# Kernel optimization log

Hardware: AMD Instinct MI355X
Metric: run time of the kernel (lower is better)

## Reference

```python
import jax, jax.numpy as jnp
import numpy as np

B, S, E, H = 4, 2048, 1024, 16
HD = E // H  # head_dim = 64


def setup_inputs() -> dict:
    key = jax.random.key(0)
    k1, k2, k3, k4 = jax.random.split(key, 4)
    x = jax.random.normal(k1, (B, S, E), dtype=jnp.float32)
    # torch Linear stores weight as (out, in); y = x @ W.T
    w_qkv = jax.random.normal(k2, (3 * E, E), dtype=jnp.float32) * (E ** -0.5)
    w_proj = jax.random.normal(k3, (E, E), dtype=jnp.float32) * (E ** -0.5)
    b_proj = jax.random.normal(k4, (E,), dtype=jnp.float32) * 0.01
    return {"x": x, "w_qkv": w_qkv, "w_proj": w_proj, "b_proj": b_proj}


def reference(x, w_qkv, w_proj, b_proj):
    b, s, e = x.shape
    # fused QKV, then per-head interleaved split (matches view(B,S,H,3*hd).chunk)
    qkv = jnp.einsum('bse,fe->bsf', x, w_qkv).reshape(b, s, H, 3 * HD)
    q, k, v = jnp.split(qkv, 3, axis=-1)  # each (b, s, H, HD)
    scale = HD ** -0.5
    scores = jnp.einsum('bqhd,bkhd->bhqk', q, k) * scale
    causal = jnp.tril(jnp.ones((s, s), dtype=bool))
    scores = jnp.where(causal, scores, jnp.float32(-jnp.inf))
    probs = jax.nn.softmax(scores, axis=-1)
    out = jnp.einsum('bhqk,bkhd->bqhd', probs, v).reshape(b, s, e)
    return jnp.einsum('bse,fe->bsf', out, w_proj) + b_proj
```

## Files before the change

kernel.cpp:

```cpp
#include <hip/hip_runtime.h>

#define Bq   4
#define Sq   2048
#define Eq   1024
#define Hq   16
#define HDq  64
#define Mq   (Bq*Sq)
#define N1q  (3*Eq)
#define Kq   Eq

typedef __bf16 bf16x8 __attribute__((ext_vector_type(8)));
typedef __bf16 bf16x4 __attribute__((ext_vector_type(4)));
typedef float  f32x4  __attribute__((ext_vector_type(4)));
typedef float  f32x16 __attribute__((ext_vector_type(16)));

#define GAS __attribute__((address_space(1)))
#define LAS __attribute__((address_space(3)))

__device__ __forceinline__ void gl2lds16(const void* g, void* l) {
  __builtin_amdgcn_global_load_lds((GAS const void*)g, (LAS void*)l, 16, 0, 0);
}

__device__ __forceinline__ unsigned pack2(float a, float b) {
  union { __bf16 h[2]; unsigned u; } x;
  x.h[0] = (__bf16)a; x.h[1] = (__bf16)b; return x.u;
}

__global__ __launch_bounds__(256) void cvt4(const float* __restrict__ in,
                                            __bf16* __restrict__ out, int n4) {
  int i = blockIdx.x * 256 + threadIdx.x;
  if (i >= n4) return;
  float4 v = ((const float4*)in)[i];
  bf16x4 o = { (__bf16)v.x, (__bf16)v.y, (__bf16)v.z, (__bf16)v.w };
  ((bf16x4*)out)[i] = o;
}

template <int MODE>
__global__ __launch_bounds__(256) void gemm_bt(const __bf16* __restrict__ A,
                                               const __bf16* __restrict__ Bw,
                                               int N, int K,
                                               __bf16* __restrict__ cbf,
                                               const float* __restrict__ bias,
                                               float* __restrict__ cf32) {
  __shared__ __align__(16) __bf16 As[128 * 32];
  __shared__ __align__(16) __bf16 Bs[128 * 32];
  const int tid  = threadIdx.x;
  const int wave = tid >> 6, lane = tid & 63;
  const int quad = lane >> 4, l15 = lane & 15;
  const int wm = wave & 1, wn = wave >> 1;
  const int bm0 = blockIdx.x * 128;
  const int bn0 = blockIdx.y * 128;

  f32x4 acc[4][4] = {};

  const int ar = tid >> 2, ac = (tid & 3) * 8;
  const __bf16* Ag0 = A  + (long)(bm0 + ar) * K + ac;
  const __bf16* Bg0 = Bw + (long)(bn0 + ar) * K + ac;
  __bf16* As0 = As + wave * 512; __bf16* As1 = As + 2048 + wave * 512;
  __bf16* Bs0 = Bs + wave * 512; __bf16* Bs1 = Bs + 2048 + wave * 512;

  for (int kc = 0; kc < K; kc += 32) {
    gl2lds16(Ag0 + kc,          As0);
    gl2lds16(Ag0 + 64 * K + kc, As1);
    gl2lds16(Bg0 + kc,          Bs0);
    gl2lds16(Bg0 + 64 * K + kc, Bs1);
    __syncthreads();

    bf16x8 af[4], bfr[4];
#pragma unroll
    for (int mt = 0; mt < 4; mt++)
      af[mt] = *(const bf16x8*)&As[(wm * 64 + mt * 16 + l15) * 32 + quad * 8];
#pragma unroll
    for (int nt = 0; nt < 4; nt++)
      bfr[nt] = *(const bf16x8*)&Bs[(wn * 64 + nt * 16 + l15) * 32 + quad * 8];
#pragma unroll
    for (int mt = 0; mt < 4; mt++)
#pragma unroll
      for (int nt = 0; nt < 4; nt++)
        acc[mt][nt] = __builtin_amdgcn_mfma_f32_16x16x32_bf16(af[mt], bfr[nt], acc[mt][nt], 0, 0, 0);
    __syncthreads();
  }

#pragma unroll
  for (int nt = 0; nt < 4; nt++) {
    const int n = bn0 + wn * 64 + nt * 16 + l15;
    float bv = 0.f;
    if (MODE == 1) bv = bias[n];
#pragma unroll
    for (int mt = 0; mt < 4; mt++) {
      const int mbase = bm0 + wm * 64 + mt * 16 + quad * 4;
#pragma unroll
      for (int r = 0; r < 4; r++) {
        const long m = mbase + r;
        if (MODE == 0) cbf[m * N + n] = (__bf16)acc[mt][nt][r];
        else           cf32[m * N + n] = acc[mt][nt][r] + bv;
      }
    }
  }
}

__global__ __launch_bounds__(256) void transv(const __bf16* __restrict__ qkv,
                                              __bf16* __restrict__ vt) {
  __shared__ __align__(16) __bf16 T[64 * 64];
  const int tid = threadIdx.x, wave = tid >> 6;
  const int bh = blockIdx.x >> 5, st = blockIdx.x & 31;
  const int b = bh >> 4, h = bh & 15;
  const long gbase = (long)(b * Sq + st * 64 + (tid >> 3)) * N1q + h * 192 + 128 + (tid & 7) * 8;
  gl2lds16(qkv + gbase,                  T + wave * 512);
  gl2lds16(qkv + gbase + (long)32 * N1q, T + 2048 + wave * 512);
  __syncthreads();
  const int d = tid >> 2, s4 = (tid & 3) * 16;
  bf16x8 o0, o1;
#pragma unroll
  for (int j = 0; j < 8; j++) o0[j] = T[(s4 + j) * 64 + d];
#pragma unroll
  for (int j = 0; j < 8; j++) o1[j] = T[(s4 + 8 + j) * 64 + d];
  __bf16* dst = vt + (long)(bh * 64 + d) * Sq + st * 64 + s4;
  *(bf16x8*)dst = o0;
  *(bf16x8*)(dst + 8) = o1;
}

__global__ __launch_bounds__(256, 2) void attn_fwd(const __bf16* __restrict__ qkv,
                                                   const __bf16* __restrict__ vt,
                                                   __bf16* __restrict__ aout) {
  __shared__ __align__(16) __bf16 Ks[128 * 64];
  __shared__ __align__(16) __bf16 Vs[64 * 128];

  const int tid = threadIdx.x;
  const int w = tid >> 6, lane = tid & 63;
  const int c = lane & 31, h = lane >> 5;
  const int bh = blockIdx.x & 63, p = blockIdx.x >> 6;
  const int b = bh >> 4, head = bh & 15;

  const int krr = lane >> 3, kj = lane & 7;
  const int vrr = lane >> 4, vj = lane & 15;
  constexpr float SC2 = 0.18033688011112042f;

  for (int which = 0; which < 2; ++which) {
    const int qt = which ? (15 - p) : p;
    const int q_g = qt * 128 + w * 32 + c;

    bf16x8 qf[4];
    const __bf16* qp = qkv + (long)(b * Sq + q_g) * N1q + head * 192 + h * 8;
#pragma unroll
    for (int kc2 = 0; kc2 < 4; kc2++) qf[kc2] = *(const bf16x8*)(qp + kc2 * 16);

    f32x16 oT[2] = {};
    float m_i = -1e30f, l_i = 0.f;

    const int nk = qt + 1;
    for (int kt = 0; kt < nk; kt++) {
#pragma unroll
      for (int i = 0; i < 4; i++) {
        const int row = w * 32 + i * 8 + krr;
        gl2lds16(qkv + (long)(b * Sq + kt * 128 + row) * N1q + head * 192 + 64
                     + (kj ^ (krr & 7)) * 8,
                 Ks + (w * 32 + i * 8) * 64);
      }
#pragma unroll
      for (int i = 0; i < 4; i++) {
        const int dr = w * 16 + i * 4 + vrr;
        gl2lds16(vt + (long)(bh * 64 + dr) * Sq + kt * 128 + (vj ^ (dr & 7)) * 8,
                 Vs + (w * 16 + i * 4) * 128);
      }
      __syncthreads();

      f32x16 S[4];
#pragma unroll
      for (int nf = 0; nf < 4; nf++) {
        f32x16 z = {};
#pragma unroll
        for (int kc2 = 0; kc2 < 4; kc2++) {
          bf16x8 kf = *(const bf16x8*)&Ks[(nf * 32 + c) * 64 + (((kc2 * 2 + h) ^ (c & 7)) * 8)];
          z = __builtin_amdgcn_mfma_f32_32x32x16_bf16(kf, qf[kc2], z, 0, 0, 0);
        }
        S[nf] = z;
      }

      float mx = -1e30f;
      if (kt == qt) {
#pragma unroll
        for (int nf = 0; nf < 4; nf++)
#pragma unroll
          for (int r = 0; r < 16; r++) {
            const int kcol = kt * 128 + nf * 32 + (r & 3) + 8 * (r >> 2) + 4 * h;
            float s = S[nf][r] * SC2;
            s = (kcol > q_g) ? -1e30f : s;
            S[nf][r] = s; mx = fmaxf(mx, s);
          }
      } else {
#pragma unroll
        for (int nf = 0; nf < 4; nf++)
#pragma unroll
          for (int r = 0; r < 16; r++) {
            float s = S[nf][r] * SC2;
            S[nf][r] = s; mx = fmaxf(mx, s);
          }
      }
      mx = fmaxf(mx, __shfl_xor(mx, 32));
      const float mn = fmaxf(m_i, mx);
      const float alpha = exp2f(m_i - mn);
      m_i = mn;
      float sum = 0.f;
#pragma unroll
      for (int nf = 0; nf < 4; nf++)
#pragma unroll
        for (int r = 0; r < 16; r++) {
          float pv = exp2f(S[nf][r] - mn);
          S[nf][r] = pv; sum += pv;
        }
      sum += __shfl_xor(sum, 32);
      l_i = l_i * alpha + sum;
      oT[0] *= alpha; oT[1] *= alpha;

#pragma unroll
      for (int kc = 0; kc < 8; kc++) {
        const int nf = kc >> 1, base = 8 * (kc & 1);
        const unsigned pa0 = pack2(S[nf][base + 0], S[nf][base + 1]);
        const unsigned pa1 = pack2(S[nf][base + 2], S[nf][base + 3]);
        const unsigned pb0 = pack2(S[nf][base + 4], S[nf][base + 5]);
        const unsigned pb1 = pack2(S[nf][base + 6], S[nf][base + 7]);
        const unsigned ou0 = h ? pb0 : pa0, ou1 = h ? pb1 : pa1;
        const unsigned su0 = h ? pa0 : pb0, su1 = h ? pa1 : pb1;
        const unsigned ru0 = __shfl_xor(su0, 32), ru1 = __shfl_xor(su1, 32);
        union { bf16x8 v; unsigned u[4]; } pf;
        pf.u[0] = h ? ru0 : ou0;
        pf.u[1] = h ? ru1 : ou1;
        pf.u[2] = h ? ou0 : ru0;
        pf.u[3] = h ? ou1 : ru1;
#pragma unroll
        for (int nf2 = 0; nf2 < 2; nf2++) {
          bf16x8 vf = *(const bf16x8*)&Vs[(nf2 * 32 + c) * 128 + (((kc * 2 + h) ^ (c & 7)) * 8)];
          oT[nf2] = __builtin_amdgcn_mfma_f32_32x32x16_bf16(vf, pf.v, oT[nf2], 0, 0, 0);
        }
      }
      __syncthreads();
    }

    const float inv = 1.0f / l_i;
    const long obase = (long)(b * Sq + q_g) * Eq + head * 64;
#pragma unroll
    for (int nf2 = 0; nf2 < 2; nf2++)
#pragma unroll
      for (int g = 0; g < 4; g++) {
        bf16x4 o;
#pragma unroll
        for (int t = 0; t < 4; t++) o[t] = (__bf16)(oT[nf2][g * 4 + t] * inv);
        *(bf16x4*)(aout + obase + nf2 * 32 + 8 * g + 4 * h) = o;
      }
  }
}

extern "C" void kernel_launch(void* const* d_in, const int* in_sizes, int n_in,
                              void* d_out, int out_size, void* d_ws, size_t ws_size,
                              hipStream_t stream) {
  const float* x      = (const float*)d_in[0];
  const float* w_qkv  = (const float*)d_in[1];
  const float* w_proj = (const float*)d_in[2];
  const float* b_proj = (const float*)d_in[3];
  float* out = (float*)d_out;

  char* w = (char*)d_ws;
  __bf16* xb     = (__bf16*)w; w += (size_t)Mq * Kq * 2;
  __bf16* wqkvb  = (__bf16*)w; w += (size_t)N1q * Kq * 2;
  __bf16* wprojb = (__bf16*)w; w += (size_t)Eq * Kq * 2;
  __bf16* qkvb   = (__bf16*)w; w += (size_t)Mq * N1q * 2;
  __bf16* vtb    = (__bf16*)w; w += (size_t)Bq * Hq * HDq * Sq * 2;
  __bf16* attnb  = (__bf16*)w;

  cvt4<<<(Mq * Kq / 4 + 255) / 256, 256, 0, stream>>>(x, xb, Mq * Kq / 4);
  cvt4<<<(N1q * Kq / 4 + 255) / 256, 256, 0, stream>>>(w_qkv, wqkvb, N1q * Kq / 4);
  cvt4<<<(Eq * Kq / 4 + 255) / 256, 256, 0, stream>>>(w_proj, wprojb, Eq * Kq / 4);

  gemm_bt<0><<<dim3(Mq / 128, N1q / 128), 256, 0, stream>>>(xb, wqkvb, N1q, Kq, qkvb, nullptr, nullptr);

  transv<<<Bq * Hq * (Sq / 64), 256, 0, stream>>>(qkvb, vtb);

  attn_fwd<<<64 * 8, 256, 0, stream>>>(qkvb, vtb, attnb);

  gemm_bt<1><<<dim3(Mq / 128, Eq / 128), 256, 0, stream>>>(attnb, wprojb, Eq, Kq, nullptr, b_proj, out);
}
```

Measured before the change: 292.6 us.

## Fold softmax scale into Q weights and launch one attention block per query tile

Scales the Q rows of the QKV weight during the fp32-to-bf16 conversion by the softmax scale times log2(e), which removes the per-score multiply inside the attention loop. The attention kernel now launches one block per query tile (1024 blocks) instead of pairing tiles p and 15-p in one block, and launch bounds allow 4 blocks per CU. The max and sum reductions are split into two chains for more ILP, and the P-fragment shuffle selection is simplified. The risks are load imbalance from causal tiles of very different lengths, register pressure under the tighter launch bound, and slightly different rounding because Q is scaled before the bf16 cast.

New measurement: 347.7 us. 18.8% more time.

```diff
diff --git a/kernel.cpp b/kernel.cpp
--- a/kernel.cpp
+++ b/kernel.cpp
@@ -32,6 +32,18 @@
   if (i >= n4) return;
   float4 v = ((const float4*)in)[i];
   bf16x4 o = { (__bf16)v.x, (__bf16)v.y, (__bf16)v.z, (__bf16)v.w };
+  ((bf16x4*)out)[i] = o;
+}
+
+__global__ __launch_bounds__(256) void cvt_wqkv(const float* __restrict__ in,
+                                                __bf16* __restrict__ out, int n4) {
+  int i = blockIdx.x * 256 + threadIdx.x;
+  if (i >= n4) return;
+  const int f = i >> 8;
+  const float sc = ((f % 192) < 64) ? 0.18033688011112042f : 1.0f;
+  float4 v = ((const float4*)in)[i];
+  bf16x4 o = { (__bf16)(v.x * sc), (__bf16)(v.y * sc),
+               (__bf16)(v.z * sc), (__bf16)(v.w * sc) };
   ((bf16x4*)out)[i] = o;
 }
 
@@ -120,7 +132,7 @@
   *(bf16x8*)(dst + 8) = o1;
 }
 
-__global__ __launch_bounds__(256, 2) void attn_fwd(const __bf16* __restrict__ qkv,
+__global__ __launch_bounds__(256, 4) void attn_fwd(const __bf16* __restrict__ qkv,
                                                    const __bf16* __restrict__ vt,
                                                    __bf16* __restrict__ aout) {
   __shared__ __align__(16) __bf16 Ks[128 * 64];
@@ -129,126 +141,121 @@
   const int tid = threadIdx.x;
   const int w = tid >> 6, lane = tid & 63;
   const int c = lane & 31, h = lane >> 5;
-  const int bh = blockIdx.x & 63, p = blockIdx.x >> 6;
+  const int bh = blockIdx.x & 63, qt = blockIdx.x >> 6;
   const int b = bh >> 4, head = bh & 15;
 
   const int krr = lane >> 3, kj = lane & 7;
   const int vrr = lane >> 4, vj = lane & 15;
-  constexpr float SC2 = 0.18033688011112042f;
-
-  for (int which = 0; which < 2; ++which) {
-    const int qt = which ? (15 - p) : p;
-    const int q_g = qt * 128 + w * 32 + c;
-
-    bf16x8 qf[4];
-    const __bf16* qp = qkv + (long)(b * Sq + q_g) * N1q + head * 192 + h * 8;
-#pragma unroll
-    for (int kc2 = 0; kc2 < 4; kc2++) qf[kc2] = *(const bf16x8*)(qp + kc2 * 16);
-
-    f32x16 oT[2] = {};
-    float m_i = -1e30f, l_i = 0.f;
-
-    const int nk = qt + 1;
-    for (int kt = 0; kt < nk; kt++) {
-#pragma unroll
-      for (int i = 0; i < 4; i++) {
-        const int row = w * 32 + i * 8 + krr;
-        gl2lds16(qkv + (long)(b * Sq + kt * 128 + row) * N1q + head * 192 + 64
-                     + (kj ^ (krr & 7)) * 8,
-                 Ks + (w * 32 + i * 8) * 64);
-      }
-#pragma unroll
-      for (int i = 0; i < 4; i++) {
-        const int dr = w * 16 + i * 4 + vrr;
-        gl2lds16(vt + (long)(bh * 64 + dr) * Sq + kt * 128 + (vj ^ (dr & 7)) * 8,
-                 Vs + (w * 16 + i * 4) * 128);
-      }
-      __syncthreads();
-
-      f32x16 S[4];
-#pragma unroll
-      for (int nf = 0; nf < 4; nf++) {
-        f32x16 z = {};
-#pragma unroll
-        for (int kc2 = 0; kc2 < 4; kc2++) {
-          bf16x8 kf = *(const bf16x8*)&Ks[(nf * 32 + c) * 64 + (((kc2 * 2 + h) ^ (c & 7)) * 8)];
-          z = __builtin_amdgcn_mfma_f32_32x32x16_bf16(kf, qf[kc2], z, 0, 0, 0);
+
+  const int q_g = qt * 128 + w * 32 + c;
+
+  bf16x8 qf[4];
+  const __bf16* qp = qkv + (long)(b * Sq + q_g) * N1q + head * 192 + h * 8;
+#pragma unroll
+  for (int kc2 = 0; kc2 < 4; kc2++) qf[kc2] = *(const bf16x8*)(qp + kc2 * 16);
+
+  f32x16 oT[2] = {};
+  float m_i = -1e30f, l_i = 0.f;
+
+  const int nk = qt + 1;
+  for (int kt = 0; kt < nk; kt++) {
+#pragma unroll
+    for (int i = 0; i < 4; i++) {
+      const int row = w * 32 + i * 8 + krr;
+      gl2lds16(qkv + (long)(b * Sq + kt * 128 + row) * N1q + head * 192 + 64
+                   + (kj ^ (krr & 7)) * 8,
+               Ks + (w * 32 + i * 8) * 64);
+    }
+#pragma unroll
+    for (int i = 0; i < 4; i++) {
+      const int dr = w * 16 + i * 4 + vrr;
+      gl2lds16(vt + (long)(bh * 64 + dr) * Sq + kt * 128 + (vj ^ (dr & 7)) * 8,
+               Vs + (w * 16 + i * 4) * 128);
+    }
+    __syncthreads();
+
+    f32x16 S[4];
+#pragma unroll
+    for (int nf = 0; nf < 4; nf++) {
+      f32x16 z = {};
+#pragma unroll
+      for (int kc2 = 0; kc2 < 4; kc2++) {
+        bf16x8 kf = *(const bf16x8*)&Ks[(nf * 32 + c) * 64 + (((kc2 * 2 + h) ^ (c & 7)) * 8)];
+        z = __builtin_amdgcn_mfma_f32_32x32x16_bf16(kf, qf[kc2], z, 0, 0, 0);
+      }
+      S[nf] = z;
+    }
+
+    if (kt == qt) {
+#pragma unroll
+      for (int nf = 0; nf < 4; nf++)
+#pragma unroll
+        for (int r = 0; r < 16; r++) {
+          const int kcol = kt * 128 + nf * 32 + (r & 3) + 8 * (r >> 2) + 4 * h;
+          if (kcol > q_g) S[nf][r] = -1e30f;
         }
-        S[nf] = z;
-      }
-
-      float mx = -1e30f;
-      if (kt == qt) {
-#pragma unroll
-        for (int nf = 0; nf < 4; nf++)
-#pragma unroll
-          for (int r = 0; r < 16; r++) {
-            const int kcol = kt * 128 + nf * 32 + (r & 3) + 8 * (r >> 2) + 4 * h;
-            float s = S[nf][r] * SC2;
-            s = (kcol > q_g) ? -1e30f : s;
-            S[nf][r] = s; mx = fmaxf(mx, s);
-          }
-      } else {
-#pragma unroll
-        for (int nf = 0; nf < 4; nf++)
-#pragma unroll
-          for (int r = 0; r < 16; r++) {
-            float s = S[nf][r] * SC2;
-            S[nf][r] = s; mx = fmaxf(mx, s);
-          }
-      }
-      mx = fmaxf(mx, __shfl_xor(mx, 32));
-      const float mn = fmaxf(m_i, mx);
-      const float alpha = exp2f(m_i - mn);
-      m_i = mn;
-      float sum = 0.f;
-#pragma unroll
-      for (int nf = 0; nf < 4; nf++)
-#pragma unroll
-        for (int r = 0; r < 16; r++) {
-          float pv = exp2f(S[nf][r] - mn);
-          S[nf][r] = pv; sum += pv;
-        }
-      sum += __shfl_xor(sum, 32);
-      l_i = l_i * alpha + sum;
-      oT[0] *= alpha; oT[1] *= alpha;
-
-#pragma unroll
-      for (int kc = 0; kc < 8; kc++) {
-        const int nf = kc >> 1, base = 8 * (kc & 1);
-        const unsigned pa0 = pack2(S[nf][base + 0], S[nf][base + 1]);
-        const unsigned pa1 = pack2(S[nf][base + 2], S[nf][base + 3]);
-        const unsigned pb0 = pack2(S[nf][base + 4], S[nf][base + 5]);
-        const unsigned pb1 = pack2(S[nf][base + 6], S[nf][base + 7]);
-        const unsigned ou0 = h ? pb0 : pa0, ou1 = h ? pb1 : pa1;
-        const unsigned su0 = h ? pa0 : pb0, su1 = h ? pa1 : pb1;
-        const unsigned ru0 = __shfl_xor(su0, 32), ru1 = __shfl_xor(su1, 32);
-        union { bf16x8 v; unsigned u[4]; } pf;
-        pf.u[0] = h ? ru0 : ou0;
-        pf.u[1] = h ? ru1 : ou1;
-        pf.u[2] = h ? ou0 : ru0;
-        pf.u[3] = h ? ou1 : ru1;
-#pragma unroll
-        for (int nf2 = 0; nf2 < 2; nf2++) {
-          bf16x8 vf = *(const bf16x8*)&Vs[(nf2 * 32 + c) * 128 + (((kc * 2 + h) ^ (c & 7)) * 8)];
-          oT[nf2] = __builtin_amdgcn_mfma_f32_32x32x16_bf16(vf, pf.v, oT[nf2], 0, 0, 0);
-        }
-      }
-      __syncthreads();
-    }
-
-    const float inv = 1.0f / l_i;
-    const long obase = (long)(b * Sq + q_g) * Eq + head * 64;
-#pragma unroll
-    for (int nf2 = 0; nf2 < 2; nf2++)
-#pragma unroll
-      for (int g = 0; g < 4; g++) {
-        bf16x4 o;
-#pragma unroll
-        for (int t = 0; t < 4; t++) o[t] = (__bf16)(oT[nf2][g * 4 + t] * inv);
-        *(bf16x4*)(aout + obase + nf2 * 32 + 8 * g + 4 * h) = o;
-      }
+    }
+    float mx = -1e30f;
+#pragma unroll
+    for (int nf = 0; nf < 4; nf++)
+#pragma unroll
+      for (int r = 0; r < 16; r += 2)
+        mx = fmaxf(fmaxf(mx, S[nf][r]), S[nf][r + 1]);
+    mx = fmaxf(mx, __shfl_xor(mx, 32));
+    const float mn = fmaxf(m_i, mx);
+    const float alpha = exp2f(m_i - mn);
+    m_i = mn;
+    float s0 = 0.f, s1 = 0.f;
+#pragma unroll
+    for (int nf = 0; nf < 4; nf++)
+#pragma unroll
+      for (int r = 0; r < 16; r += 2) {
+        float p0 = exp2f(S[nf][r] - mn);
+        float p1 = exp2f(S[nf][r + 1] - mn);
+        S[nf][r] = p0; S[nf][r + 1] = p1;
+        s0 += p0; s1 += p1;
+      }
+    float sum = s0 + s1;
+    sum += __shfl_xor(sum, 32);
+    l_i = l_i * alpha + sum;
+    oT[0] *= alpha; oT[1] *= alpha;
+
+#pragma unroll
+    for (int kc = 0; kc < 8; kc++) {
+      const int nf = kc >> 1, base = 8 * (kc & 1);
+      const unsigned pa0 = pack2(S[nf][base + 0], S[nf][base + 1]);
+      const unsigned pa1 = pack2(S[nf][base + 2], S[nf][base + 3]);
+      const unsigned pb0 = pack2(S[nf][base + 4], S[nf][base + 5]);
+      const unsigned pb1 = pack2(S[nf][base + 6], S[nf][base + 7]);
+      const unsigned send0 = h ? pa0 : pb0;
+      const unsigned send1 = h ? pa1 : pb1;
+      const unsigned recv0 = __shfl_xor(send0, 32);
+      const unsigned recv1 = __shfl_xor(send1, 32);
+      union { bf16x8 v; unsigned u[4]; } pf;
+      pf.u[0] = h ? recv0 : pa0;
+      pf.u[1] = h ? recv1 : pa1;
+      pf.u[2] = h ? pb0 : recv0;
+      pf.u[3] = h ? pb1 : recv1;
+#pragma unroll
+      for (int nf2 = 0; nf2 < 2; nf2++) {
+        bf16x8 vf = *(const bf16x8*)&Vs[(nf2 * 32 + c) * 128 + (((kc * 2 + h) ^ (c & 7)) * 8)];
+        oT[nf2] = __builtin_amdgcn_mfma_f32_32x32x16_bf16(vf, pf.v, oT[nf2], 0, 0, 0);
+      }
+    }
+    __syncthreads();
   }
+
+  const float inv = 1.0f / l_i;
+  const long obase = (long)(b * Sq + q_g) * Eq + head * 64;
+#pragma unroll
+  for (int nf2 = 0; nf2 < 2; nf2++)
+#pragma unroll
+    for (int g = 0; g < 4; g++) {
+      bf16x4 o;
+#pragma unroll
+      for (int t = 0; t < 4; t++) o[t] = (__bf16)(oT[nf2][g * 4 + t] * inv);
+      *(bf16x4*)(aout + obase + nf2 * 32 + 8 * g + 4 * h) = o;
+    }
 }
 
 extern "C" void kernel_launch(void* const* d_in, const int* in_sizes, int n_in,
@@ -269,14 +276,14 @@
   __bf16* attnb  = (__bf16*)w;
 
   cvt4<<<(Mq * Kq / 4 + 255) / 256, 256, 0, stream>>>(x, xb, Mq * Kq / 4);
-  cvt4<<<(N1q * Kq / 4 + 255) / 256, 256, 0, stream>>>(w_qkv, wqkvb, N1q * Kq / 4);
+  cvt_wqkv<<<(N1q * Kq / 4 + 255) / 256, 256, 0, stream>>>(w_qkv, wqkvb, N1q * Kq / 4);
   cvt4<<<(Eq * Kq / 4 + 255) / 256, 256, 0, stream>>>(w_proj, wprojb, Eq * Kq / 4);
 
   gemm_bt<0><<<dim3(Mq / 128, N1q / 128), 256, 0, stream>>>(xb, wqkvb, N1q, Kq, qkvb, nullptr, nullptr);
 
   transv<<<Bq * Hq * (Sq / 64), 256, 0, stream>>>(qkvb, vtb);
 
-  attn_fwd<<<64 * 8, 256, 0, stream>>>(qkvb, vtb, attnb);
+  attn_fwd<<<16 * 64, 256, 0, stream>>>(qkvb, vtb, attnb);
 
   gemm_bt<1><<<dim3(Mq / 128, Eq / 128), 256, 0, stream>>>(attnb, wprojb, Eq, Kq, nullptr, b_proj, out);
 }
```
